# Kernel optimization log

Measured on AMD Instinct MI355X. Metric: run time of the kernel, lower is better.

## Reference

```python
import jax, jax.numpy as jnp
import numpy as np

N, D_MODEL, D_PE, H = 4096, 512, 16, 8


def setup_inputs() -> dict:
    key = jax.random.key(0)
    ks = jax.random.split(key, 6)
    s = 1.0 / np.sqrt(D_MODEL)
    return {
        "x": jax.random.normal(ks[0], (N, D_MODEL), dtype=jnp.float32),
        "pe": jax.random.normal(ks[1], (N, D_PE), dtype=jnp.float32),
        "w_qkv": jax.random.normal(ks[2], (D_MODEL, 3 * D_MODEL), dtype=jnp.float32) * s,
        "b_qkv": jnp.zeros((3 * D_MODEL,), dtype=jnp.float32),
        "w_pe": jax.random.normal(ks[3], (D_PE, H), dtype=jnp.float32) * (1.0 / np.sqrt(D_PE)),
        "b_pe": jnp.zeros((H,), dtype=jnp.float32),
        "w_out": jax.random.normal(ks[4], (D_MODEL, D_MODEL), dtype=jnp.float32) * s,
        "b_out": jnp.zeros((D_MODEL,), dtype=jnp.float32),
    }


def reference(x, pe, w_qkv, b_qkv, w_pe, b_pe, w_out, b_out):
    n, d = x.shape
    h = w_pe.shape[1]
    hd = d // h
    scale = hd ** -0.5

    qkv = (x @ w_qkv + b_qkv).reshape(n, 3, h, hd)  # [N,3,H,hd]
    q = jnp.transpose(qkv[:, 0], (1, 0, 2))  # [H,N,hd]
    k = jnp.transpose(qkv[:, 1], (1, 0, 2))
    v = jnp.transpose(qkv[:, 2], (1, 0, 2))

    pe_proj = pe @ w_pe + b_pe  # [N,H]
    # bias[h,i,j] = pe_proj[j,h] - pe_proj[i,h]  (matches torch unsqueeze/permute)
    pt = pe_proj.T  # [H,N]
    bias = pt[:, None, :] - pt[:, :, None]  # [H,N,N]

    scores = jnp.einsum('hnd,hmd->hnm', q, k) * scale + bias  # [H,N,N]
    attn = jax.nn.softmax(scores, axis=-1)
    out = jnp.einsum('hnm,hmd->hnd', attn, v)  # [H,N,hd]
    out = jnp.transpose(out, (1, 0, 2)).reshape(n, d)
    return out @ w_out + b_out
```

## Files before the change

kernel.cpp:

```cpp
#include <hip/hip_runtime.h>
#include <stdint.h>
#include <stddef.h>


typedef unsigned short u16;
typedef __attribute__((ext_vector_type(8))) short short8;
typedef __attribute__((ext_vector_type(8))) unsigned short us8;
typedef __attribute__((ext_vector_type(4))) unsigned short us4;
typedef __attribute__((ext_vector_type(4))) float floatx4;

__device__ __forceinline__ u16 f2b(float f) {
  union { float f; uint32_t u; } v; v.f = f;
  uint32_t u = v.u;
  return (u16)((u + 0x7fffu + ((u >> 16) & 1u)) >> 16);
}

__device__ __forceinline__ uint32_t pkbf16(float a, float b) {
  union { float f; uint32_t u; } x, y; x.f = a; y.f = b;
  return __builtin_amdgcn_perm(y.u + 0x8000u, x.u + 0x8000u, 0x07060302u);
}

#if __has_builtin(__builtin_amdgcn_exp2f)
__device__ __forceinline__ float fexp2(float x) { return __builtin_amdgcn_exp2f(x); }
#else
__device__ __forceinline__ float fexp2(float x) { return exp2f(x); }
#endif

__device__ __forceinline__ void gld16(const u16* g, u16* l) {
  __builtin_amdgcn_global_load_lds(
      (const __attribute__((address_space(1))) uint32_t*)(const void*)g,
      (__attribute__((address_space(3))) uint32_t*)(void*)l, 16, 0, 0);
}


__device__ __forceinline__ void tr_tile(const float* __restrict__ in,
                                        u16* __restrict__ out, int R, int C,
                                        int bx, int by, u16 (*tile)[33]) {
  int tx = threadIdx.x & 31, ty = threadIdx.x >> 5;
  int c0 = bx * 32, r0 = by * 32;
#pragma unroll
  for (int i = 0; i < 32; i += 8)
    tile[ty + i][tx] = f2b(in[(size_t)(r0 + ty + i) * C + c0 + tx]);
  __syncthreads();
#pragma unroll
  for (int i = 0; i < 32; i += 8)
    out[(size_t)(c0 + ty + i) * R + r0 + tx] = tile[tx][ty + i];
}

__global__ __launch_bounds__(256) void k_prep(
    const float* __restrict__ x, u16* __restrict__ xb,
    const float* __restrict__ w_qkv, u16* __restrict__ wqkvT,
    const float* __restrict__ w_out, u16* __restrict__ woutT,
    const float* __restrict__ pe, const float* __restrict__ w_pe,
    const float* __restrict__ b_pe, float* __restrict__ wexp,
    u16* __restrict__ wpb) {
  __shared__ u16 tile[32][33];
  int b = blockIdx.x;
  if (b < 2048) {
    int i = b * 256 + threadIdx.x;
    float4 v = ((const float4*)x)[i];
    uint2 o = make_uint2(pkbf16(v.x, v.y), pkbf16(v.z, v.w));
    ((uint2*)xb)[i] = o;
  } else if (b < 2816) {
    int idx = b - 2048;
    tr_tile(w_qkv, wqkvT, 512, 1536, idx % 48, idx / 48, tile);
  } else if (b < 3072) {
    int idx = b - 2816;
    tr_tile(w_out, woutT, 512, 512, idx % 16, idx / 16, tile);
  } else {
    int idx = (b - 3072) * 256 + threadIdx.x;
    int h = idx >> 12, n = idx & 4095;
    float acc = b_pe[h];
#pragma unroll
    for (int d = 0; d < 16; ++d) acc = fmaf(pe[n * 16 + d], w_pe[d * 8 + h], acc);
    float w = exp2f(acc * 1.4426950408889634f - 16.0f);
    u16 wb = f2b(w);
    union { uint32_t u; float f; } cv; cv.u = ((uint32_t)wb) << 16;
    wexp[h * 4096 + n] = cv.f;
    int pn = (n & ~31) | (((n >> 2) & 3) << 3) | (((n >> 4) & 1) << 2) | (n & 3);
    wpb[h * 4096 + pn] = wb;
  }
}


__global__ __launch_bounds__(512, 6) void k_gemm_qkv(const u16* __restrict__ A,
                                                     const u16* __restrict__ Bt,
                                                     const float* __restrict__ bias,
                                                     const float* __restrict__ wexp,
                                                     u16* __restrict__ qk,
                                                     u16* __restrict__ vtp) {
  __shared__ __align__(16) u16 smem[24576];
  const int tid = threadIdx.x;
  const int lane = tid & 63, wave = tid >> 6;
  const int colx = lane & 15, quad = lane >> 4;
  const int m0 = blockIdx.y * 64, n0 = blockIdx.x * 128;
  const int wm = wave >> 2, wn = wave & 3;
  const int sc = (lane & 7) ^ ((lane >> 3) & 7);
  const floatx4 fz = {0.f, 0.f, 0.f, 0.f};
  floatx4 acc[2][2];
#pragma unroll
  for (int i = 0; i < 2; ++i)
#pragma unroll
    for (int j = 0; j < 2; ++j) acc[i][j] = fz;

#define PREF_QKV(k0, b)                                                       \
  {                                                                           \
    int rowa = wave * 8 + (lane >> 3);                                        \
    gld16(&A[(size_t)(m0 + rowa) * 512 + (k0) + sc * 8],                      \
          &smem[(b) * 4096 + wave * 512 + lane * 8]);                         \
    _Pragma("unroll") for (int c = 0; c < 2; ++c) {                           \
      int rowb = wave * 16 + c * 8 + (lane >> 3);                             \
      gld16(&Bt[(size_t)(n0 + rowb) * 512 + (k0) + sc * 8],                   \
            &smem[8192 + (b) * 8192 + wave * 1024 + c * 512 + lane * 8]);     \
    }                                                                         \
  }

  PREF_QKV(0, 0);
  __syncthreads();
  for (int it = 0; it < 8; ++it) {
    int cur = it & 1;
    if (it < 7) PREF_QKV((it + 1) * 64, cur ^ 1);
    const u16* As = &smem[cur * 4096];
    const u16* Bs = &smem[8192 + cur * 8192];
#pragma unroll
    for (int kk = 0; kk < 2; ++kk) {
      short8 af[2], bf[2];
#pragma unroll
      for (int i = 0; i < 2; ++i) {
        int row = wm * 32 + i * 16 + colx;
        af[i] = *(const short8*)&As[row * 64 + (((kk * 4 + quad) ^ (colx & 7))) * 8];
      }
#pragma unroll
      for (int j = 0; j < 2; ++j) {
        int row = wn * 32 + j * 16 + colx;
        bf[j] = *(const short8*)&Bs[row * 64 + (((kk * 4 + quad) ^ (colx & 7))) * 8];
      }
#pragma unroll
      for (int i = 0; i < 2; ++i)
#pragma unroll
        for (int j = 0; j < 2; ++j)
          acc[i][j] = __builtin_amdgcn_mfma_f32_16x16x32_bf16(af[i], bf[j], acc[i][j], 0, 0, 0);
    }
    __syncthreads();
  }

  const bool isV = (blockIdx.x >= 8);
  if (!isV) {
#pragma unroll
    for (int j = 0; j < 2; ++j) {
      int c = n0 + wn * 32 + j * 16 + colx;
      float bq = bias[c];
      float qs = (c < 512) ? 0.18033688011112042f : 1.0f;
#pragma unroll
      for (int i = 0; i < 2; ++i)
#pragma unroll
        for (int r = 0; r < 4; ++r) {
          int row = m0 + wm * 32 + i * 16 + quad * 4 + r;
          qk[(size_t)row * 1024 + c] = f2b((acc[i][j][r] + bq) * qs);
        }
    }
  } else {
    const int dv = n0 - 1024;
    u16* Vl = smem;
    const int hh = (dv + wn * 32) >> 6;
#pragma unroll
    for (int j = 0; j < 2; ++j) {
      float bq = bias[n0 + wn * 32 + j * 16 + colx];
#pragma unroll
      for (int i = 0; i < 2; ++i) {
        floatx4 wv = *(const floatx4*)&wexp[hh * 4096 + m0 + wm * 32 + i * 16 + quad * 4];
        us4 o;
#pragma unroll
        for (int r = 0; r < 4; ++r) o[r] = f2b((acc[i][j][r] + bq) * wv[r]);
        int dl = wn * 32 + j * 16 + colx;
        int nc = wm * 32 + quad * 8 + i * 4;
        *(us4*)&Vl[dl * 72 + nc] = o;
      }
    }
    __syncthreads();
#pragma unroll
    for (int t = 0; t < 2; ++t) {
      int idx = t * 512 + tid;
      int dl = idx >> 3, ch = idx & 7;
      *(us8*)&vtp[(size_t)(dv + dl) * 4096 + m0 + ch * 8] =
          *(const us8*)&Vl[dl * 72 + ch * 8];
    }
  }
#undef PREF_QKV
}


__global__ __launch_bounds__(256, 4) void k_flash(const u16* __restrict__ qk,
                                                  const u16* __restrict__ vt,
                                                  const u16* __restrict__ wpb,
                                                  float* __restrict__ opart,
                                                  float* __restrict__ lpart) {
  __shared__ __align__(16) u16 smem[16384];
  float* bufs = (float*)smem;

  const int tid = threadIdx.x;
  const int lane = tid & 63, wave = tid >> 6;
  const int colx = lane & 15, quad = lane >> 4;
  const int ih = wave >> 1, jq = wave & 1;
  const int q0 = blockIdx.x * 64;
  const int h = blockIdx.y;
  const int z = blockIdx.z;
  const int kvb = z * 2048;
  const floatx4 fz = {0.f, 0.f, 0.f, 0.f};

  const int sc = (lane & 7) ^ ((lane >> 3) & 7);
  const int srow = wave * 16 + (lane >> 3);

  const u16* qptr = qk + (size_t)(kvb + srow) * 1024 + 512 + h * 64 + sc * 8;
  const u16* vptr = vt + (size_t)(h * 64 + srow) * 4096 + kvb + sc * 8;
  const u16* wptr = wpb + h * 4096 + kvb + jq * 32 + quad * 8;
  gld16(qptr, &smem[wave * 1024 + lane * 8]);
  gld16(qptr + 8192, &smem[wave * 1024 + 512 + lane * 8]);
  gld16(vptr, &smem[8192 + wave * 1024 + lane * 8]);
  gld16(vptr + 32768, &smem[8192 + wave * 1024 + 512 + lane * 8]);
  qptr += 65536;
  vptr += 64;

  short8 qf[2][2];
#pragma unroll
  for (int iq = 0; iq < 2; ++iq)
#pragma unroll
    for (int kk = 0; kk < 2; ++kk) {
      int row = q0 + ih * 32 + iq * 16 + colx;
      qf[iq][kk] = *(const short8*)&qk[(size_t)row * 1024 + h * 64 + (kk * 4 + quad) * 8];
    }
  __syncthreads();

  floatx4 oacc[2][4], lacc[2];
  lacc[0] = fz; lacc[1] = fz;
#pragma unroll
  for (int iq = 0; iq < 2; ++iq)
#pragma unroll
    for (int cb = 0; cb < 4; ++cb) oacc[iq][cb] = fz;

#define FBODY(CUR, PREF)                                                      \
  {                                                                           \
    short8 wf = *(const short8*)wptr;                                         \
    wptr += 64;                                                               \
    asm volatile("" ::: "memory");   \
    if (PREF) {                                                               \
      gld16(qptr, &smem[(1 - (CUR)) * 4096 + wave * 1024 + lane * 8]);        \
      gld16(qptr + 8192,                                                      \
            &smem[(1 - (CUR)) * 4096 + wave * 1024 + 512 + lane * 8]);        \
      gld16(vptr, &smem[8192 + (1 - (CUR)) * 4096 + wave * 1024 + lane * 8]); \
      gld16(vptr + 32768,                                                     \
            &smem[8192 + (1 - (CUR)) * 4096 + wave * 1024 + 512 + lane * 8]); \
      qptr += 65536;                                                          \
      vptr += 64;                                                             \
         \
      asm volatile("s_waitcnt vmcnt(4)" ::: "memory");                        \
    } else {                                                                  \
      asm volatile("s_waitcnt vmcnt(0)" ::: "memory");                        \
    }                                                                         \
    __builtin_amdgcn_s_barrier();                                             \
    asm volatile("" ::: "memory");  \
    const u16* Ks = &smem[(CUR) * 4096];                                      \
    const u16* Vts = &smem[8192 + (CUR) * 4096];                              \
    floatx4 sacc[2][2] = {{fz, fz}, {fz, fz}};                                \
    _Pragma("unroll") for (int j2 = 0; j2 < 2; ++j2) {                        \
      _Pragma("unroll") for (int kk = 0; kk < 2; ++kk) {                      \
        int row = jq * 32 + j2 * 16 + colx;                                   \
        short8 kf = *(const short8*)&Ks[row * 64 +                            \
                                        (((kk * 4 + quad) ^ (colx & 7))) * 8];\
        sacc[0][j2] = __builtin_amdgcn_mfma_f32_16x16x32_bf16(                \
            kf, qf[0][kk], sacc[0][j2], 0, 0, 0);                             \
        sacc[1][j2] = __builtin_amdgcn_mfma_f32_16x16x32_bf16(                \
            kf, qf[1][kk], sacc[1][j2], 0, 0, 0);                             \
      }                                                                       \
    }                                                                         \
    union { uint32_t w[4]; short8 s; } pk[2];                                 \
    _Pragma("unroll") for (int iq = 0; iq < 2; ++iq) {                        \
      _Pragma("unroll") for (int j2 = 0; j2 < 2; ++j2) {                      \
        float p0 = fexp2(sacc[iq][j2][0]);                                    \
        float p1 = fexp2(sacc[iq][j2][1]);                                    \
        float p2 = fexp2(sacc[iq][j2][2]);                                    \
        float p3 = fexp2(sacc[iq][j2][3]);                                    \
        pk[iq].w[j2 * 2 + 0] = pkbf16(p0, p1);                                \
        pk[iq].w[j2 * 2 + 1] = pkbf16(p2, p3);                                \
      }                                                                       \
    }                                                                         \
    _Pragma("unroll") for (int cb = 0; cb < 4; ++cb) {                        \
      int row = cb * 16 + colx;                                               \
      short8 vf = *(const short8*)&Vts[row * 64 +                             \
                                       (((jq * 4 + quad) ^ (colx & 7))) * 8]; \
      oacc[0][cb] = __builtin_amdgcn_mfma_f32_16x16x32_bf16(                  \
          pk[0].s, vf, oacc[0][cb], 0, 0, 0);                                 \
      oacc[1][cb] = __builtin_amdgcn_mfma_f32_16x16x32_bf16(                  \
          pk[1].s, vf, oacc[1][cb], 0, 0, 0);                                 \
    }                                                                         \
    lacc[0] = __builtin_amdgcn_mfma_f32_16x16x32_bf16(pk[0].s, wf, lacc[0], 0, 0, 0); \
    lacc[1] = __builtin_amdgcn_mfma_f32_16x16x32_bf16(pk[1].s, wf, lacc[1], 0, 0, 0); \
    asm volatile("" ::: "memory");   \
    __builtin_amdgcn_s_barrier();                                             \
    asm volatile("" ::: "memory");     \
  }

  for (int t = 0; t < 15; ++t) {
    FBODY(0, 1)
    FBODY(1, 1)
  }
  FBODY(0, 1)
  FBODY(1, 0)
#undef FBODY

  float* b = bufs + ih * 2080;
  if (jq == 1) {
#pragma unroll
    for (int iq = 0; iq < 2; ++iq)
#pragma unroll
      for (int cb = 0; cb < 4; ++cb)
#pragma unroll
        for (int r = 0; r < 4; ++r)
          b[(iq * 16 + quad * 4 + r) * 65 + cb * 16 + colx] = oacc[iq][cb][r];
    if (colx == 0)
#pragma unroll
      for (int iq = 0; iq < 2; ++iq)
#pragma unroll
        for (int r = 0; r < 4; ++r) b[(iq * 16 + quad * 4 + r) * 65 + 64] = lacc[iq][r];
  }
  __syncthreads();
  if (jq == 0) {
#pragma unroll
    for (int iq = 0; iq < 2; ++iq) {
#pragma unroll
      for (int cb = 0; cb < 4; ++cb)
#pragma unroll
        for (int r = 0; r < 4; ++r)
          oacc[iq][cb][r] += b[(iq * 16 + quad * 4 + r) * 65 + cb * 16 + colx];
#pragma unroll
      for (int r = 0; r < 4; ++r) lacc[iq][r] += b[(iq * 16 + quad * 4 + r) * 65 + 64];
    }
    float* op = opart + (size_t)z * 2097152;
#pragma unroll
    for (int iq = 0; iq < 2; ++iq)
#pragma unroll
      for (int cb = 0; cb < 4; ++cb)
#pragma unroll
        for (int r = 0; r < 4; ++r)
          op[(size_t)(q0 + ih * 32 + iq * 16 + quad * 4 + r) * 512 + h * 64 + cb * 16 + colx] =
              oacc[iq][cb][r];
    if (colx == 0)
#pragma unroll
      for (int iq = 0; iq < 2; ++iq)
#pragma unroll
        for (int r = 0; r < 4; ++r)
          lpart[z * 32768 + h * 4096 + q0 + ih * 32 + iq * 16 + quad * 4 + r] = lacc[iq][r];
  }
}


__global__ __launch_bounds__(256) void k_comb(const float* __restrict__ opart,
                                              const float* __restrict__ lpart,
                                              u16* __restrict__ ao) {
  int idx = blockIdx.x * 256 + threadIdx.x;
  int n = idx >> 7, d4 = idx & 127;
  int h = d4 >> 4;
  float l = lpart[h * 4096 + n] + lpart[32768 + h * 4096 + n];
  float inv = 1.0f / l;
  float4 o0 = *(const float4*)&opart[(size_t)n * 512 + d4 * 4];
  float4 o1 = *(const float4*)&opart[2097152 + (size_t)n * 512 + d4 * 4];
  us4 o;
  o[0] = f2b((o0.x + o1.x) * inv);
  o[1] = f2b((o0.y + o1.y) * inv);
  o[2] = f2b((o0.z + o1.z) * inv);
  o[3] = f2b((o0.w + o1.w) * inv);
  *(us4*)&ao[(size_t)n * 512 + d4 * 4] = o;
}


__global__ __launch_bounds__(512, 4) void k_gemm_out(const u16* __restrict__ A,
                                                     const u16* __restrict__ Bt,
                                                     const float* __restrict__ bias,
                                                     float* __restrict__ Cout) {
  __shared__ __align__(16) u16 smem[16384];
  const int tid = threadIdx.x;
  const int lane = tid & 63, wave = tid >> 6;
  const int colx = lane & 15, quad = lane >> 4;
  const int m0 = blockIdx.y * 64, n0 = blockIdx.x * 64;
  const int wm = wave >> 2, wn = wave & 3;
  const int sc = (lane & 7) ^ ((lane >> 3) & 7);
  const floatx4 fz = {0.f, 0.f, 0.f, 0.f};
  floatx4 acc[2];
  acc[0] = fz; acc[1] = fz;

#define PREF_OUT(k0, b)                                                       \
  {                                                                           \
    int rowa = wave * 8 + (lane >> 3);                                        \
    gld16(&A[(size_t)(m0 + rowa) * 512 + (k0) + sc * 8],                      \
          &smem[(b) * 4096 + wave * 512 + lane * 8]);                         \
    gld16(&Bt[(size_t)(n0 + rowa) * 512 + (k0) + sc * 8],                     \
          &smem[8192 + (b) * 4096 + wave * 512 + lane * 8]);                  \
  }

  PREF_OUT(0, 0);
  __syncthreads();
  for (int it = 0; it < 8; ++it) {
    int cur = it & 1;
    if (it < 7) PREF_OUT((it + 1) * 64, cur ^ 1);
    const u16* As = &smem[cur * 4096];
    const u16* Bs = &smem[8192 + cur * 4096];
#pragma unroll
    for (int kk = 0; kk < 2; ++kk) {
      short8 af[2], bf;
#pragma unroll
      for (int i = 0; i < 2; ++i) {
        int row = wm * 32 + i * 16 + colx;
        af[i] = *(const short8*)&As[row * 64 + (((kk * 4 + quad) ^ (colx & 7))) * 8];
      }
      {
        int row = wn * 16 + colx;
        bf = *(const short8*)&Bs[row * 64 + (((kk * 4 + quad) ^ (colx & 7))) * 8];
      }
#pragma unroll
      for (int i = 0; i < 2; ++i)
        acc[i] = __builtin_amdgcn_mfma_f32_16x16x32_bf16(af[i], bf, acc[i], 0, 0, 0);
    }
    __syncthreads();
  }
  int c = n0 + wn * 16 + colx;
  float bq = bias[c];
#pragma unroll
  for (int i = 0; i < 2; ++i)
#pragma unroll
    for (int r = 0; r < 4; ++r) {
      int row = m0 + wm * 32 + i * 16 + quad * 4 + r;
      Cout[(size_t)row * 512 + c] = acc[i][r] + bq;
    }
#undef PREF_OUT
}


extern "C" void kernel_launch(void* const* d_in, const int* in_sizes, int n_in,
                              void* d_out, int out_size, void* d_ws, size_t ws_size,
                              hipStream_t stream) {
  const float* x     = (const float*)d_in[0];
  const float* pe    = (const float*)d_in[1];
  const float* w_qkv = (const float*)d_in[2];
  const float* b_qkv = (const float*)d_in[3];
  const float* w_pe  = (const float*)d_in[4];
  const float* b_pe  = (const float*)d_in[5];
  const float* w_out = (const float*)d_in[6];
  const float* b_out = (const float*)d_in[7];
  float* out = (float*)d_out;

  u16* xb    = (u16*)d_ws;
  u16* wqkvT = xb    + 2097152;
  u16* woutT = wqkvT + 786432;
  u16* qk    = woutT + 262144;
  u16* vt    = qk    + 4194304;
  u16* wpb   = vt    + 2097152;
  u16* ao    = wpb   + 32768;
  float* wexp  = (float*)(ao + 2097152);
  float* opart = wexp + 32768;
  float* lpart = opart + 4194304;

  k_prep<<<3200, 256, 0, stream>>>(x, xb, w_qkv, wqkvT, w_out, woutT,
                                   pe, w_pe, b_pe, wexp, wpb);
  k_gemm_qkv<<<dim3(12, 64), 512, 0, stream>>>(xb, wqkvT, b_qkv, wexp, qk, vt);
  k_flash<<<dim3(64, 8, 2), 256, 0, stream>>>(qk, vt, wpb, opart, lpart);
  k_comb<<<2048, 256, 0, stream>>>(opart, lpart, ao);
  k_gemm_out<<<dim3(8, 64), 512, 0, stream>>>(ao, woutT, b_out, out);
}
```

Baseline: 141.4 us.

## Software-pipeline PV matmul one tile behind QK to overlap exp with MFMA

Restructures the flash-attention inner loop so the P·V and row-sum MFMAs for the previous tile run at the start of the next iteration, interleaved with the QK^T MFMAs of the current tile. V fragments, packed probabilities and the weight fragment are kept in registers across iterations, with a prologue and epilogue added. The aim is to hide exp/pack latency and LDS read latency behind independent MFMA work. The vmcnt wait is adjusted for the extra outstanding load, and an explicit lgkmcnt(0) is added before the barrier. In exchange it raises register pressure.

```diff
diff --git a/kernel.cpp b/kernel.cpp
--- a/kernel.cpp
+++ b/kernel.cpp
@@ -238,11 +238,15 @@
 #pragma unroll
     for (int cb = 0; cb < 4; ++cb) oacc[iq][cb] = fz;
 
-#define FBODY(CUR, PREF)                                                      \
+  union { uint32_t w[4]; short8 s; } pkp[2];
+  short8 vfr[4];
+  short8 wfp;
+
+#define FBODY(CUR, PREF, DOPV)                                                \
   {                                                                           \
-    short8 wf = *(const short8*)wptr;                                         \
+    short8 wfn = *(const short8*)wptr;                                        \
     wptr += 64;                                                               \
-    asm volatile("" ::: "memory");   \
+    asm volatile("" ::: "memory");  \
     if (PREF) {                                                               \
       gld16(qptr, &smem[(1 - (CUR)) * 4096 + wave * 1024 + lane * 8]);        \
       gld16(qptr + 8192,                                                      \
@@ -252,8 +256,8 @@
             &smem[8192 + (1 - (CUR)) * 4096 + wave * 1024 + 512 + lane * 8]); \
       qptr += 65536;                                                          \
       vptr += 64;                                                             \
-         \
-      asm volatile("s_waitcnt vmcnt(4)" ::: "memory");                        \
+             \
+      asm volatile("s_waitcnt vmcnt(5)" ::: "memory");                        \
     } else {                                                                  \
       asm volatile("s_waitcnt vmcnt(0)" ::: "memory");                        \
     }                                                                         \
@@ -261,52 +265,67 @@
     asm volatile("" ::: "memory");  \
     const u16* Ks = &smem[(CUR) * 4096];                                      \
     const u16* Vts = &smem[8192 + (CUR) * 4096];                              \
-    floatx4 sacc[2][2] = {{fz, fz}, {fz, fz}};                                \
-    _Pragma("unroll") for (int j2 = 0; j2 < 2; ++j2) {                        \
+    short8 kf[2][2];                                                          \
+    _Pragma("unroll") for (int j2 = 0; j2 < 2; ++j2)                          \
       _Pragma("unroll") for (int kk = 0; kk < 2; ++kk) {                      \
         int row = jq * 32 + j2 * 16 + colx;                                   \
-        short8 kf = *(const short8*)&Ks[row * 64 +                            \
-                                        (((kk * 4 + quad) ^ (colx & 7))) * 8];\
+        kf[j2][kk] = *(const short8*)&Ks[row * 64 +                           \
+                                         (((kk * 4 + quad) ^ (colx & 7))) * 8]; \
+      }                                                                       \
+    if (DOPV) {       \
+      _Pragma("unroll") for (int cb = 0; cb < 4; ++cb) {                      \
+        oacc[0][cb] = __builtin_amdgcn_mfma_f32_16x16x32_bf16(                \
+            pkp[0].s, vfr[cb], oacc[0][cb], 0, 0, 0);                         \
+        oacc[1][cb] = __builtin_amdgcn_mfma_f32_16x16x32_bf16(                \
+            pkp[1].s, vfr[cb], oacc[1][cb], 0, 0, 0);                         \
+      }                                                                       \
+      lacc[0] = __builtin_amdgcn_mfma_f32_16x16x32_bf16(pkp[0].s, wfp, lacc[0], 0, 0, 0); \
+      lacc[1] = __builtin_amdgcn_mfma_f32_16x16x32_bf16(pkp[1].s, wfp, lacc[1], 0, 0, 0); \
+    }                                                                         \
+    floatx4 sacc[2][2] = {{fz, fz}, {fz, fz}};                                \
+    _Pragma("unroll") for (int j2 = 0; j2 < 2; ++j2)                          \
+      _Pragma("unroll") for (int kk = 0; kk < 2; ++kk) {                      \
         sacc[0][j2] = __builtin_amdgcn_mfma_f32_16x16x32_bf16(                \
-            kf, qf[0][kk], sacc[0][j2], 0, 0, 0);                             \
+            kf[j2][kk], qf[0][kk], sacc[0][j2], 0, 0, 0);                     \
         sacc[1][j2] = __builtin_amdgcn_mfma_f32_16x16x32_bf16(                \
-            kf, qf[1][kk], sacc[1][j2], 0, 0, 0);                             \
+            kf[j2][kk], qf[1][kk], sacc[1][j2], 0, 0, 0);                     \
       }                                                                       \
+    _Pragma("unroll") for (int cb = 0; cb < 4; ++cb) {                        \
+      int row = cb * 16 + colx;                                               \
+      vfr[cb] = *(const short8*)&Vts[row * 64 +                               \
+                                     (((jq * 4 + quad) ^ (colx & 7))) * 8];   \
     }                                                                         \
-    union { uint32_t w[4]; short8 s; } pk[2];                                 \
-    _Pragma("unroll") for (int iq = 0; iq < 2; ++iq) {                        \
+    _Pragma("unroll") for (int iq = 0; iq < 2; ++iq)                          \
       _Pragma("unroll") for (int j2 = 0; j2 < 2; ++j2) {                      \
         float p0 = fexp2(sacc[iq][j2][0]);                                    \
         float p1 = fexp2(sacc[iq][j2][1]);                                    \
         float p2 = fexp2(sacc[iq][j2][2]);                                    \
         float p3 = fexp2(sacc[iq][j2][3]);                                    \
-        pk[iq].w[j2 * 2 + 0] = pkbf16(p0, p1);                                \
-        pk[iq].w[j2 * 2 + 1] = pkbf16(p2, p3);                                \
+        pkp[iq].w[j2 * 2 + 0] = pkbf16(p0, p1);                               \
+        pkp[iq].w[j2 * 2 + 1] = pkbf16(p2, p3);                               \
       }                                                                       \
-    }                                                                         \
-    _Pragma("unroll") for (int cb = 0; cb < 4; ++cb) {                        \
-      int row = cb * 16 + colx;                                               \
-      short8 vf = *(const short8*)&Vts[row * 64 +                             \
-                                       (((jq * 4 + quad) ^ (colx & 7))) * 8]; \
-      oacc[0][cb] = __builtin_amdgcn_mfma_f32_16x16x32_bf16(                  \
-          pk[0].s, vf, oacc[0][cb], 0, 0, 0);                                 \
-      oacc[1][cb] = __builtin_amdgcn_mfma_f32_16x16x32_bf16(                  \
-          pk[1].s, vf, oacc[1][cb], 0, 0, 0);                                 \
-    }                                                                         \
-    lacc[0] = __builtin_amdgcn_mfma_f32_16x16x32_bf16(pk[0].s, wf, lacc[0], 0, 0, 0); \
-    lacc[1] = __builtin_amdgcn_mfma_f32_16x16x32_bf16(pk[1].s, wf, lacc[1], 0, 0, 0); \
-    asm volatile("" ::: "memory");   \
+    wfp = wfn;                                                                \
+            \
+    asm volatile("s_waitcnt lgkmcnt(0)" ::: "memory");                        \
     __builtin_amdgcn_s_barrier();                                             \
     asm volatile("" ::: "memory");     \
   }
 
+  FBODY(0, 1, 0)
   for (int t = 0; t < 15; ++t) {
-    FBODY(0, 1)
-    FBODY(1, 1)
-  }
-  FBODY(0, 1)
-  FBODY(1, 0)
+    FBODY(1, 1, 1)
+    FBODY(0, 1, 1)
+  }
+  FBODY(1, 0, 1)
 #undef FBODY
+
+#pragma unroll
+  for (int cb = 0; cb < 4; ++cb) {
+    oacc[0][cb] = __builtin_amdgcn_mfma_f32_16x16x32_bf16(pkp[0].s, vfr[cb], oacc[0][cb], 0, 0, 0);
+    oacc[1][cb] = __builtin_amdgcn_mfma_f32_16x16x32_bf16(pkp[1].s, vfr[cb], oacc[1][cb], 0, 0, 0);
+  }
+  lacc[0] = __builtin_amdgcn_mfma_f32_16x16x32_bf16(pkp[0].s, wfp, lacc[0], 0, 0, 0);
+  lacc[1] = __builtin_amdgcn_mfma_f32_16x16x32_bf16(pkp[1].s, wfp, lacc[1], 0, 0, 0);
 
   float* b = bufs + ih * 2080;
   if (jq == 1) {
```

Measured after the change: 155.9 us. +10.3%, slower.

## Triple-buffer K/V tiles in LDS and drop per-iteration trailing barrier

Applied to the files above, without the earlier changes.

Expands the K/V shared-memory staging from two to three buffers, so each iteration needs only one barrier instead of two. The positional-bias weight fragment is now loaded one iteration ahead into registers, and the wait counts are adjusted to match. MFMA phases are wrapped with s_setprio to favour the matrix work over other waves. Shared memory per block grows to 48 KB, which may lower how many blocks fit on each CU compared with the launch-bounds target of 4.

```diff
diff --git a/kernel.cpp b/kernel.cpp
--- a/kernel.cpp
+++ b/kernel.cpp
@@ -195,7 +195,7 @@
                                                   const u16* __restrict__ wpb,
                                                   float* __restrict__ opart,
                                                   float* __restrict__ lpart) {
-  __shared__ __align__(16) u16 smem[16384];
+  __shared__ __align__(16) u16 smem[24576];
   float* bufs = (float*)smem;
 
   const int tid = threadIdx.x;
@@ -216,8 +216,8 @@
   const u16* wptr = wpb + h * 4096 + kvb + jq * 32 + quad * 8;
   gld16(qptr, &smem[wave * 1024 + lane * 8]);
   gld16(qptr + 8192, &smem[wave * 1024 + 512 + lane * 8]);
-  gld16(vptr, &smem[8192 + wave * 1024 + lane * 8]);
-  gld16(vptr + 32768, &smem[8192 + wave * 1024 + 512 + lane * 8]);
+  gld16(vptr, &smem[12288 + wave * 1024 + lane * 8]);
+  gld16(vptr + 32768, &smem[12288 + wave * 1024 + 512 + lane * 8]);
   qptr += 65536;
   vptr += 64;
 
@@ -229,7 +229,8 @@
       int row = q0 + ih * 32 + iq * 16 + colx;
       qf[iq][kk] = *(const short8*)&qk[(size_t)row * 1024 + h * 64 + (kk * 4 + quad) * 8];
     }
-  __syncthreads();
+  short8 wfp = *(const short8*)wptr;
+  wptr += 64;
 
   floatx4 oacc[2][4], lacc[2];
   lacc[0] = fz; lacc[1] = fz;
@@ -238,30 +239,35 @@
 #pragma unroll
     for (int cb = 0; cb < 4; ++cb) oacc[iq][cb] = fz;
 
-#define FBODY(CUR, PREF)                                                      \
+#define PB0 1
+#define PB1 2
+#define PB2 0
+#define FBODY(B, PBX, PREF)                                                   \
   {                                                                           \
-    short8 wf = *(const short8*)wptr;                                         \
-    wptr += 64;                                                               \
-    asm volatile("" ::: "memory");   \
+    short8 wfn;                                                               \
     if (PREF) {                                                               \
-      gld16(qptr, &smem[(1 - (CUR)) * 4096 + wave * 1024 + lane * 8]);        \
+      wfn = *(const short8*)wptr;                    \
+      wptr += 64;                                                             \
+      asm volatile("" ::: "memory");                                          \
+      gld16(qptr, &smem[(PBX) * 4096 + wave * 1024 + lane * 8]);              \
       gld16(qptr + 8192,                                                      \
-            &smem[(1 - (CUR)) * 4096 + wave * 1024 + 512 + lane * 8]);        \
-      gld16(vptr, &smem[8192 + (1 - (CUR)) * 4096 + wave * 1024 + lane * 8]); \
+            &smem[(PBX) * 4096 + wave * 1024 + 512 + lane * 8]);              \
+      gld16(vptr, &smem[12288 + (PBX) * 4096 + wave * 1024 + lane * 8]);      \
       gld16(vptr + 32768,                                                     \
-            &smem[8192 + (1 - (CUR)) * 4096 + wave * 1024 + 512 + lane * 8]); \
+            &smem[12288 + (PBX) * 4096 + wave * 1024 + 512 + lane * 8]);      \
       qptr += 65536;                                                          \
       vptr += 64;                                                             \
-         \
-      asm volatile("s_waitcnt vmcnt(4)" ::: "memory");                        \
+              \
+      asm volatile("s_waitcnt vmcnt(5)" ::: "memory");                        \
     } else {                                                                  \
       asm volatile("s_waitcnt vmcnt(0)" ::: "memory");                        \
     }                                                                         \
     __builtin_amdgcn_s_barrier();                                             \
     asm volatile("" ::: "memory");  \
-    const u16* Ks = &smem[(CUR) * 4096];                                      \
-    const u16* Vts = &smem[8192 + (CUR) * 4096];                              \
+    const u16* Ks = &smem[(B) * 4096];                                        \
+    const u16* Vts = &smem[12288 + (B) * 4096];                               \
     floatx4 sacc[2][2] = {{fz, fz}, {fz, fz}};                                \
+    __builtin_amdgcn_s_setprio(1);                                            \
     _Pragma("unroll") for (int j2 = 0; j2 < 2; ++j2) {                        \
       _Pragma("unroll") for (int kk = 0; kk < 2; ++kk) {                      \
         int row = jq * 32 + j2 * 16 + colx;                                   \
@@ -273,6 +279,7 @@
             kf, qf[1][kk], sacc[1][j2], 0, 0, 0);                             \
       }                                                                       \
     }                                                                         \
+    __builtin_amdgcn_s_setprio(0);                                            \
     union { uint32_t w[4]; short8 s; } pk[2];                                 \
     _Pragma("unroll") for (int iq = 0; iq < 2; ++iq) {                        \
       _Pragma("unroll") for (int j2 = 0; j2 < 2; ++j2) {                      \
@@ -284,6 +291,7 @@
         pk[iq].w[j2 * 2 + 1] = pkbf16(p2, p3);                                \
       }                                                                       \
     }                                                                         \
+    __builtin_amdgcn_s_setprio(1);                                            \
     _Pragma("unroll") for (int cb = 0; cb < 4; ++cb) {                        \
       int row = cb * 16 + colx;                                               \
       short8 vf = *(const short8*)&Vts[row * 64 +                             \
@@ -293,20 +301,26 @@
       oacc[1][cb] = __builtin_amdgcn_mfma_f32_16x16x32_bf16(                  \
           pk[1].s, vf, oacc[1][cb], 0, 0, 0);                                 \
     }                                                                         \
-    lacc[0] = __builtin_amdgcn_mfma_f32_16x16x32_bf16(pk[0].s, wf, lacc[0], 0, 0, 0); \
-    lacc[1] = __builtin_amdgcn_mfma_f32_16x16x32_bf16(pk[1].s, wf, lacc[1], 0, 0, 0); \
+    lacc[0] = __builtin_amdgcn_mfma_f32_16x16x32_bf16(pk[0].s, wfp, lacc[0], 0, 0, 0); \
+    lacc[1] = __builtin_amdgcn_mfma_f32_16x16x32_bf16(pk[1].s, wfp, lacc[1], 0, 0, 0); \
+    __builtin_amdgcn_s_setprio(0);                                            \
+    if (PREF) wfp = wfn;                                                      \
     asm volatile("" ::: "memory");   \
-    __builtin_amdgcn_s_barrier();                                             \
-    asm volatile("" ::: "memory");     \
-  }
-
-  for (int t = 0; t < 15; ++t) {
-    FBODY(0, 1)
-    FBODY(1, 1)
-  }
-  FBODY(0, 1)
-  FBODY(1, 0)
+  }
+
+  FBODY(0, PB0, 1)
+  for (int t = 0; t < 10; ++t) {
+    FBODY(1, PB1, 1)
+    FBODY(2, PB2, 1)
+    FBODY(0, PB0, 1)
+  }
+  FBODY(1, PB1, 0)
 #undef FBODY
+#undef PB0
+#undef PB1
+#undef PB2
+
+  __syncthreads();
 
   float* b = bufs + ih * 2080;
   if (jq == 1) {
```

New measurement: 148.8 us. 1.05x slower.
